# Kernel optimization log

Hardware: AMD Instinct MI355X
Metric: run time of the kernel (lower is better)

The kernel has to match this reference:

```python
import jax, jax.numpy as jnp
import numpy as np

N_NODES = 100000
N_EDGES = 600000
HIDDEN = 128
ALPHA = 0.1
K_HOPS = 10


def setup_inputs() -> dict:
    key = jax.random.key(0)
    k1, k2, k3, k4 = jax.random.split(key, 4)
    x = jax.random.normal(k1, (N_NODES, HIDDEN), dtype=jnp.float32)
    edge_index = jax.random.randint(k2, (2, N_EDGES), 0, N_NODES, dtype=jnp.int64)
    W = jax.random.normal(k3, (HIDDEN, HIDDEN), dtype=jnp.float32) * (1.0 / np.sqrt(HIDDEN))
    b = jax.random.normal(k4, (HIDDEN,), dtype=jnp.float32) * 0.01
    return {"x": x, "edge_index": edge_index, "W": W, "b": b}


def reference(x, edge_index, W, b):
    N = x.shape[0]
    # Linear projection (PyTorch convention: y = x W^T + b)
    h = x @ W.T + b

    # gcn_norm with added self-loops (PyG APPNPConv default)
    loop = jnp.arange(N, dtype=edge_index.dtype)
    src = jnp.concatenate([edge_index[0], loop])  # [E+N]
    dst = jnp.concatenate([edge_index[1], loop])
    ones = jnp.ones(src.shape[0], dtype=h.dtype)
    deg = jax.ops.segment_sum(ones, dst, num_segments=N)  # in-degree incl. self-loop
    dinv = jnp.where(deg > 0, jax.lax.rsqrt(deg), 0.0)
    norm = dinv[src] * dinv[dst]  # [E+N]

    # APPNP propagation: h <- (1-alpha) * A_hat h + alpha * h0
    h0 = h
    for _ in range(K_HOPS):
        msg = norm[:, None] * h[src]  # gather + scale
        agg = jax.ops.segment_sum(msg, dst, num_segments=N)  # scatter-add
        h = (1.0 - ALPHA) * agg + ALPHA * h0
    return h
```

## Files before the change

kernel.cpp:

```cpp
#include <hip/hip_runtime.h>

#define N_NODES_C 100000
#define N_EDGES_C 600000
#define HIDDEN_C 128
#define K_HOPS_C 10
#define SCAN_B 98

typedef short short8 __attribute__((ext_vector_type(8)));
typedef float f32x16 __attribute__((ext_vector_type(16)));

__device__ __forceinline__ unsigned short f2bf(float f) {
    unsigned u = __float_as_uint(f);
    return (unsigned short)((u + 0x7FFFu + ((u >> 16) & 1u)) >> 16);
}
__device__ __forceinline__ float bf_lo(unsigned p) { return __uint_as_float(p << 16); }
__device__ __forceinline__ float bf_hi(unsigned p) { return __uint_as_float(p & 0xFFFF0000u); }

__global__ void k_deg(const int* __restrict__ dst, int* __restrict__ deg, int E) {
    int e = blockIdx.x * blockDim.x + threadIdx.x;
    if (e < E) atomicAdd(&deg[dst[e]], 1);
}

__global__ __launch_bounds__(1024) void k_scan_a(const int* __restrict__ deg,
                                                 int* __restrict__ offs,
                                                 int* __restrict__ blksum,
                                                 float* __restrict__ dinv,
                                                 int* __restrict__ deghist, int N) {
    __shared__ int wtot[16];
    __shared__ int lhist[64];
    int tid = threadIdx.x;
    int i = blockIdx.x * 1024 + tid;
    int lane = tid & 63;
    int wid = tid >> 6;
    if (tid < 64) lhist[tid] = 0;
    __syncthreads();
    int v = (i < N) ? deg[i] : 0;
    if (i < N) {
        dinv[i] = rsqrtf((float)(v + 1));
        atomicAdd(&lhist[v < 63 ? v : 63], 1);
    }
    int incl = v;
#pragma unroll
    for (int d = 1; d < 64; d <<= 1) {
        int t = __shfl_up(incl, (unsigned)d, 64);
        if (lane >= d) incl += t;
    }
    if (lane == 63) wtot[wid] = incl;
    __syncthreads();
    int woff = 0, btot = 0;
#pragma unroll
    for (int w = 0; w < 16; ++w) {
        int t = wtot[w];
        if (w < wid) woff += t;
        btot += t;
    }
    if (i < N) offs[i] = woff + incl - v;
    if (tid == 0) blksum[blockIdx.x] = btot;
    if (tid < 64 && lhist[tid] != 0) atomicAdd(&deghist[tid], lhist[tid]);
}

__global__ __launch_bounds__(128) void k_scan_b(const int* __restrict__ blksum,
                                                int* __restrict__ blkoff,
                                                int* __restrict__ offs,
                                                const int* __restrict__ deghist,
                                                int* __restrict__ bucketcur,
                                                int NB, int N) {
    __shared__ int wt[2];
    int t = threadIdx.x;
    int lane = t & 63;
    int w = t >> 6;
    int v = (t < NB) ? blksum[t] : 0;
    int incl = v;
#pragma unroll
    for (int d = 1; d < 64; d <<= 1) {
        int s = __shfl_up(incl, (unsigned)d, 64);
        if (lane >= d) incl += s;
    }
    if (lane == 63) wt[w] = incl;
    __syncthreads();
    int excl = incl - v + (w == 1 ? wt[0] : 0);
    if (t < NB) blkoff[t] = excl;
    if (t == 127) offs[N] = wt[0] + wt[1];
    if (w == 0) {
        int hv = deghist[lane];
        int hincl = hv;
#pragma unroll
        for (int d = 1; d < 64; d <<= 1) {
            int s = __shfl_up(hincl, (unsigned)d, 64);
            if (lane >= d) hincl += s;
        }
        bucketcur[lane] = hincl - hv;
    }
}

__global__ __launch_bounds__(1024) void k_scan_c(int* __restrict__ offs,
                                                 int* __restrict__ cursor,
                                                 const int* __restrict__ blkoff,
                                                 const int* __restrict__ deg,
                                                 int* __restrict__ bucketcur,
                                                 int* __restrict__ perm,
                                                 uint2* __restrict__ begend, int N) {
    __shared__ int lcnt[64];
    __shared__ int lbase[64];
    int tid = threadIdx.x;
    int i = blockIdx.x * 1024 + tid;
    if (tid < 64) lcnt[tid] = 0;
    __syncthreads();
    int v = 0, d = 0, b = 0, lpos = 0;
    if (i < N) {
        v = offs[i] + blkoff[blockIdx.x];
        offs[i] = v;
        cursor[i] = v;
        d = deg[i];
        b = d < 63 ? d : 63;
        lpos = atomicAdd(&lcnt[b], 1);
    }
    __syncthreads();
    if (tid < 64) lbase[tid] = (lcnt[tid] != 0) ? atomicAdd(&bucketcur[tid], lcnt[tid]) : 0;
    __syncthreads();
    if (i < N) {
        int pos = lbase[b] + lpos;
        perm[pos] = i;
        begend[pos] = make_uint2((unsigned)v, (unsigned)(v + d));
    }
}

__global__ void k_fill(const int* __restrict__ src, const int* __restrict__ dst,
                       const float* __restrict__ dinv, int* __restrict__ cursor,
                       uint2* __restrict__ csr, int E) {
    int e = blockIdx.x * blockDim.x + threadIdx.x;
    if (e < E) {
        int s = src[e], d = dst[e];
        int pos = atomicAdd(&cursor[d], 1);
        uint2 v;
        v.x = (unsigned)s;
        v.y = __float_as_uint(dinv[s] * dinv[d]);
        csr[pos] = v;
    }
}

__global__ __launch_bounds__(256) void k_gemm(const float* __restrict__ x,
                                              const float* __restrict__ W,
                                              const float* __restrict__ b,
                                              unsigned short* __restrict__ hb, int N) {
    __shared__ unsigned short Wb[HIDDEN_C * HIDDEN_C];
    int tid = threadIdx.x;
#pragma unroll
    for (int i = 0; i < 8; ++i) {
        int c = tid + 256 * i;
        int m = c >> 4;
        int g = c & 15;
        const float4* wsrc = (const float4*)W + m * 32 + g * 2;
        float4 wa = wsrc[0];
        float4 wb = wsrc[1];
        unsigned short t8[8];
        t8[0] = f2bf(wa.x); t8[1] = f2bf(wa.y); t8[2] = f2bf(wa.z); t8[3] = f2bf(wa.w);
        t8[4] = f2bf(wb.x); t8[5] = f2bf(wb.y); t8[6] = f2bf(wb.z); t8[7] = f2bf(wb.w);
        int gs = g ^ (m & 15);
        *(uint4*)&Wb[m * 128 + gs * 8] = *(const uint4*)t8;
    }
    __syncthreads();

    int lane = tid & 63;
    int wv = tid >> 6;
    int row0 = blockIdx.x * 128 + wv * 32;
    int m = lane & 31;
    int half = lane >> 5;

    int row = row0 + m;
    if (row >= N) row = N - 1;
    const float4* xrow = (const float4*)(x + (size_t)row * 128);

    f32x16 acc[4];
#pragma unroll
    for (int t = 0; t < 4; ++t)
#pragma unroll
        for (int r = 0; r < 16; ++r) acc[t][r] = 0.f;

    for (int s = 0; s < 8; ++s) {
        int kb = s * 16 + half * 8;
        float4 x0 = xrow[kb >> 2];
        float4 x1 = xrow[(kb >> 2) + 1];
        union { unsigned short u[8]; short8 v; } af;
        af.u[0] = f2bf(x0.x); af.u[1] = f2bf(x0.y); af.u[2] = f2bf(x0.z); af.u[3] = f2bf(x0.w);
        af.u[4] = f2bf(x1.x); af.u[5] = f2bf(x1.y); af.u[6] = f2bf(x1.z); af.u[7] = f2bf(x1.w);
        int g = kb >> 3;
#pragma unroll
        for (int t = 0; t < 4; ++t) {
            int r = t * 32 + m;
            short8 bfrag = *(const short8*)&Wb[r * 128 + ((g ^ (r & 15)) << 3)];
            acc[t] = __builtin_amdgcn_mfma_f32_32x32x16_bf16(af.v, bfrag, acc[t], 0, 0, 0);
        }
    }

    float bias[4];
#pragma unroll
    for (int t = 0; t < 4; ++t) bias[t] = b[t * 32 + m];
#pragma unroll
    for (int t = 0; t < 4; ++t) {
#pragma unroll
        for (int r = 0; r < 16; ++r) {
            int rrow = (r & 3) + 8 * (r >> 2) + 4 * half;
            int node = row0 + rrow;
            if (node < N) {
                float v = acc[t][r] + bias[t];
                hb[(size_t)node * 128 + t * 32 + m] = f2bf(v);
            }
        }
    }
}

__global__ __launch_bounds__(256) void k_prop(const uint4* __restrict__ hin4,
                                              const uint4* __restrict__ h04,
                                              uint4* __restrict__ hout_b,
                                              float* __restrict__ hout_f,
                                              const int* __restrict__ perm,
                                              const uint2* __restrict__ begend,
                                              const uint2* __restrict__ csr,
                                              const float* __restrict__ dinv,
                                              int N, int final_hop) {
    int tid = threadIdx.x;
    int lane = tid & 63;
    int wid = tid >> 6;
    int q = lane >> 4;
    int f = lane & 15;

    int slot = (blockIdx.x * 4 + wid) * 4 + q;
    bool valid = slot < N;

    int node = 0, beg = 0, end = 0;
    if (valid) {
        node = perm[slot];
        uint2 be = begend[slot];
        beg = (int)be.x;
        end = (int)be.y;
    }

    uint4 hq = make_uint4(0u, 0u, 0u, 0u);
    uint4 ps = make_uint4(0u, 0u, 0u, 0u);
    float ws = 0.f;
    if (valid) {
        hq = h04[(size_t)node * 16 + f];
        ps = hin4[(size_t)node * 16 + f];
        float dv = dinv[node];
        ws = dv * dv;
    }

    float acc[8];
#pragma unroll
    for (int i = 0; i < 8; ++i) acc[i] = 0.f;

    int j = beg;
#pragma unroll 2
    for (; j + 2 <= end; j += 2) {
        uint2 e0 = csr[j];
        uint2 e1 = csr[j + 1];
        uint4 p0 = hin4[(size_t)e0.x * 16 + f];
        uint4 p1 = hin4[(size_t)e1.x * 16 + f];
        float w0 = __uint_as_float(e0.y);
        float w1 = __uint_as_float(e1.y);
        acc[0] += w0 * bf_lo(p0.x); acc[1] += w0 * bf_hi(p0.x);
        acc[2] += w0 * bf_lo(p0.y); acc[3] += w0 * bf_hi(p0.y);
        acc[4] += w0 * bf_lo(p0.z); acc[5] += w0 * bf_hi(p0.z);
        acc[6] += w0 * bf_lo(p0.w); acc[7] += w0 * bf_hi(p0.w);
        acc[0] += w1 * bf_lo(p1.x); acc[1] += w1 * bf_hi(p1.x);
        acc[2] += w1 * bf_lo(p1.y); acc[3] += w1 * bf_hi(p1.y);
        acc[4] += w1 * bf_lo(p1.z); acc[5] += w1 * bf_hi(p1.z);
        acc[6] += w1 * bf_lo(p1.w); acc[7] += w1 * bf_hi(p1.w);
    }
    if (j < end) {
        uint2 e = csr[j];
        uint4 p = hin4[(size_t)e.x * 16 + f];
        float w = __uint_as_float(e.y);
        acc[0] += w * bf_lo(p.x); acc[1] += w * bf_hi(p.x);
        acc[2] += w * bf_lo(p.y); acc[3] += w * bf_hi(p.y);
        acc[4] += w * bf_lo(p.z); acc[5] += w * bf_hi(p.z);
        acc[6] += w * bf_lo(p.w); acc[7] += w * bf_hi(p.w);
    }

    acc[0] += ws * bf_lo(ps.x); acc[1] += ws * bf_hi(ps.x);
    acc[2] += ws * bf_lo(ps.y); acc[3] += ws * bf_hi(ps.y);
    acc[4] += ws * bf_lo(ps.z); acc[5] += ws * bf_hi(ps.z);
    acc[6] += ws * bf_lo(ps.w); acc[7] += ws * bf_hi(ps.w);

    if (valid) {
        float o[8];
        o[0] = 0.9f * acc[0] + 0.1f * bf_lo(hq.x);
        o[1] = 0.9f * acc[1] + 0.1f * bf_hi(hq.x);
        o[2] = 0.9f * acc[2] + 0.1f * bf_lo(hq.y);
        o[3] = 0.9f * acc[3] + 0.1f * bf_hi(hq.y);
        o[4] = 0.9f * acc[4] + 0.1f * bf_lo(hq.z);
        o[5] = 0.9f * acc[5] + 0.1f * bf_hi(hq.z);
        o[6] = 0.9f * acc[6] + 0.1f * bf_lo(hq.w);
        o[7] = 0.9f * acc[7] + 0.1f * bf_hi(hq.w);
        if (final_hop) {
            float4* dst0 = (float4*)(hout_f + (size_t)node * 128 + f * 8);
            float4 v0; v0.x = o[0]; v0.y = o[1]; v0.z = o[2]; v0.w = o[3];
            float4 v1; v1.x = o[4]; v1.y = o[5]; v1.z = o[6]; v1.w = o[7];
            dst0[0] = v0;
            dst0[1] = v1;
        } else {
            uint4 p;
            p.x = (unsigned)f2bf(o[0]) | ((unsigned)f2bf(o[1]) << 16);
            p.y = (unsigned)f2bf(o[2]) | ((unsigned)f2bf(o[3]) << 16);
            p.z = (unsigned)f2bf(o[4]) | ((unsigned)f2bf(o[5]) << 16);
            p.w = (unsigned)f2bf(o[6]) | ((unsigned)f2bf(o[7]) << 16);
            hout_b[(size_t)node * 16 + f] = p;
        }
    }
}

extern "C" void kernel_launch(void* const* d_in, const int* in_sizes, int n_in,
                              void* d_out, int out_size, void* d_ws, size_t ws_size,
                              hipStream_t stream) {
    const float* x = (const float*)d_in[0];
    const int* edge = (const int*)d_in[1];
    const float* W = (const float*)d_in[2];
    const float* b = (const float*)d_in[3];
    float* out = (float*)d_out;

    const int N = N_NODES_C;
    const int E = N_EDGES_C;
    const int* src = edge;
    const int* dst = edge + E;

    char* ws = (char*)d_ws;
    size_t off = 0;
    auto carve = [&](size_t bytes) -> void* {
        void* p = ws + off;
        off = (off + bytes + 511) & ~(size_t)511;
        return p;
    };
    unsigned short* h0b = (unsigned short*)carve((size_t)N * HIDDEN_C * 2);
    unsigned short* bA  = (unsigned short*)carve((size_t)N * HIDDEN_C * 2);
    unsigned short* bB  = (unsigned short*)carve((size_t)N * HIDDEN_C * 2);
    int*   deg     = (int*)  carve(((size_t)N + 64) * sizeof(int));
    int*   deghist = deg + N;
    float* dinv    = (float*)carve((size_t)N * sizeof(float));
    int*   offs    = (int*)  carve((size_t)(N + 1) * sizeof(int));
    int*   cursor  = (int*)  carve((size_t)N * sizeof(int));
    uint2* csr     = (uint2*)carve((size_t)E * sizeof(uint2));
    int*   blksum  = (int*)  carve((size_t)SCAN_B * sizeof(int));
    int*   blkoff  = (int*)  carve((size_t)SCAN_B * sizeof(int));
    int*   bucketcur = (int*)carve(64 * sizeof(int));
    int*   perm    = (int*)  carve((size_t)N * sizeof(int));
    uint2* begend  = (uint2*)carve((size_t)N * sizeof(uint2));
    (void)ws_size;

    hipMemsetAsync(deg, 0, ((size_t)N + 64) * sizeof(int), stream);

    int eb = (E + 255) / 256;
    k_deg<<<eb, 256, 0, stream>>>(dst, deg, E);
    k_scan_a<<<SCAN_B, 1024, 0, stream>>>(deg, offs, blksum, dinv, deghist, N);
    k_scan_b<<<1, 128, 0, stream>>>(blksum, blkoff, offs, deghist, bucketcur, SCAN_B, N);
    k_scan_c<<<SCAN_B, 1024, 0, stream>>>(offs, cursor, blkoff, deg, bucketcur, perm, begend, N);
    k_fill<<<eb, 256, 0, stream>>>(src, dst, dinv, cursor, csr, E);

    k_gemm<<<(N + 127) / 128, 256, 0, stream>>>(x, W, b, h0b, N);

    const uint4* hin = (const uint4*)h0b;
    for (int k = 0; k < K_HOPS_C; ++k) {
        int fin = (k == K_HOPS_C - 1);
        uint4* houtb = ((k & 1) == 0) ? (uint4*)bA : (uint4*)bB;
        k_prop<<<(N + 15) / 16, 256, 0, stream>>>(hin, (const uint4*)h0b,
                                                  fin ? nullptr : houtb,
                                                  fin ? out : nullptr,
                                                  perm, begend, csr, dinv, N, fin);
        hin = houtb;
    }
}
```

Baseline: 524.8 us.

## Record per-edge rank during degree count, pack node metadata, unroll gather by four

The degree-count kernel now keeps the atomic return value as each edge's rank within its destination. The CSR fill then computes positions as offs[dst]+rank, so the second round of atomics and the cursor array are no longer needed. The perm, begend and dinv reads in the propagation kernel are merged into one uint4 metadata load per node that carries the self-loop weight precomputed. The edge-gather loop now handles four edges per iteration with clamped indices and zero weights instead of a tail loop. This adds more loads in flight and a little wasted work on short rows, and it stores a 2-byte rank per edge.

Result: faster. 499.0 us, median of 2 (-4.9%).

```diff
diff --git a/kernel.cpp b/kernel.cpp
--- a/kernel.cpp
+++ b/kernel.cpp
@@ -16,9 +16,13 @@
 __device__ __forceinline__ float bf_lo(unsigned p) { return __uint_as_float(p << 16); }
 __device__ __forceinline__ float bf_hi(unsigned p) { return __uint_as_float(p & 0xFFFF0000u); }
 
-__global__ void k_deg(const int* __restrict__ dst, int* __restrict__ deg, int E) {
+__global__ void k_deg(const int* __restrict__ dst, int* __restrict__ deg,
+                      unsigned short* __restrict__ rank, int E) {
     int e = blockIdx.x * blockDim.x + threadIdx.x;
-    if (e < E) atomicAdd(&deg[dst[e]], 1);
+    if (e < E) {
+        int r = atomicAdd(&deg[dst[e]], 1);
+        rank[e] = (unsigned short)r;
+    }
 }
 
 __global__ __launch_bounds__(1024) void k_scan_a(const int* __restrict__ deg,
@@ -94,12 +98,11 @@
 }
 
 __global__ __launch_bounds__(1024) void k_scan_c(int* __restrict__ offs,
-                                                 int* __restrict__ cursor,
                                                  const int* __restrict__ blkoff,
                                                  const int* __restrict__ deg,
+                                                 const float* __restrict__ dinv,
                                                  int* __restrict__ bucketcur,
-                                                 int* __restrict__ perm,
-                                                 uint2* __restrict__ begend, int N) {
+                                                 uint4* __restrict__ meta, int N) {
     __shared__ int lcnt[64];
     __shared__ int lbase[64];
     int tid = threadIdx.x;
@@ -110,7 +113,6 @@
     if (i < N) {
         v = offs[i] + blkoff[blockIdx.x];
         offs[i] = v;
-        cursor[i] = v;
         d = deg[i];
         b = d < 63 ? d : 63;
         lpos = atomicAdd(&lcnt[b], 1);
@@ -120,18 +122,20 @@
     __syncthreads();
     if (i < N) {
         int pos = lbase[b] + lpos;
-        perm[pos] = i;
-        begend[pos] = make_uint2((unsigned)v, (unsigned)(v + d));
+        float dv = dinv[i];
+        meta[pos] = make_uint4((unsigned)v, (unsigned)(v + d), (unsigned)i,
+                               __float_as_uint(dv * dv));
     }
 }
 
 __global__ void k_fill(const int* __restrict__ src, const int* __restrict__ dst,
-                       const float* __restrict__ dinv, int* __restrict__ cursor,
+                       const unsigned short* __restrict__ rank,
+                       const float* __restrict__ dinv, const int* __restrict__ offs,
                        uint2* __restrict__ csr, int E) {
     int e = blockIdx.x * blockDim.x + threadIdx.x;
     if (e < E) {
         int s = src[e], d = dst[e];
-        int pos = atomicAdd(&cursor[d], 1);
+        int pos = offs[d] + (int)rank[e];
         uint2 v;
         v.x = (unsigned)s;
         v.y = __float_as_uint(dinv[s] * dinv[d]);
@@ -214,10 +218,8 @@
                                               const uint4* __restrict__ h04,
                                               uint4* __restrict__ hout_b,
                                               float* __restrict__ hout_f,
-                                              const int* __restrict__ perm,
-                                              const uint2* __restrict__ begend,
+                                              const uint4* __restrict__ meta,
                                               const uint2* __restrict__ csr,
-                                              const float* __restrict__ dinv,
                                               int N, int final_hop) {
     int tid = threadIdx.x;
     int lane = tid & 63;
@@ -229,36 +231,43 @@
     bool valid = slot < N;
 
     int node = 0, beg = 0, end = 0;
+    float ws = 0.f;
     if (valid) {
-        node = perm[slot];
-        uint2 be = begend[slot];
-        beg = (int)be.x;
-        end = (int)be.y;
+        uint4 m = meta[slot];
+        beg = (int)m.x;
+        end = (int)m.y;
+        node = (int)m.z;
+        ws = __uint_as_float(m.w);
     }
 
     uint4 hq = make_uint4(0u, 0u, 0u, 0u);
     uint4 ps = make_uint4(0u, 0u, 0u, 0u);
-    float ws = 0.f;
     if (valid) {
         hq = h04[(size_t)node * 16 + f];
         ps = hin4[(size_t)node * 16 + f];
-        float dv = dinv[node];
-        ws = dv * dv;
     }
 
     float acc[8];
 #pragma unroll
     for (int i = 0; i < 8; ++i) acc[i] = 0.f;
 
-    int j = beg;
 #pragma unroll 2
-    for (; j + 2 <= end; j += 2) {
+    for (int j = beg; j < end; j += 4) {
+        int j1 = (j + 1 < end) ? j + 1 : j;
+        int j2 = (j + 2 < end) ? j + 2 : j;
+        int j3 = (j + 3 < end) ? j + 3 : j;
         uint2 e0 = csr[j];
-        uint2 e1 = csr[j + 1];
+        uint2 e1 = csr[j1];
+        uint2 e2 = csr[j2];
+        uint2 e3 = csr[j3];
         uint4 p0 = hin4[(size_t)e0.x * 16 + f];
         uint4 p1 = hin4[(size_t)e1.x * 16 + f];
+        uint4 p2 = hin4[(size_t)e2.x * 16 + f];
+        uint4 p3 = hin4[(size_t)e3.x * 16 + f];
         float w0 = __uint_as_float(e0.y);
-        float w1 = __uint_as_float(e1.y);
+        float w1 = (j + 1 < end) ? __uint_as_float(e1.y) : 0.f;
+        float w2 = (j + 2 < end) ? __uint_as_float(e2.y) : 0.f;
+        float w3 = (j + 3 < end) ? __uint_as_float(e3.y) : 0.f;
         acc[0] += w0 * bf_lo(p0.x); acc[1] += w0 * bf_hi(p0.x);
         acc[2] += w0 * bf_lo(p0.y); acc[3] += w0 * bf_hi(p0.y);
         acc[4] += w0 * bf_lo(p0.z); acc[5] += w0 * bf_hi(p0.z);
@@ -267,15 +276,14 @@
         acc[2] += w1 * bf_lo(p1.y); acc[3] += w1 * bf_hi(p1.y);
         acc[4] += w1 * bf_lo(p1.z); acc[5] += w1 * bf_hi(p1.z);
         acc[6] += w1 * bf_lo(p1.w); acc[7] += w1 * bf_hi(p1.w);
-    }
-    if (j < end) {
-        uint2 e = csr[j];
-        uint4 p = hin4[(size_t)e.x * 16 + f];
-        float w = __uint_as_float(e.y);
-        acc[0] += w * bf_lo(p.x); acc[1] += w * bf_hi(p.x);
-        acc[2] += w * bf_lo(p.y); acc[3] += w * bf_hi(p.y);
-        acc[4] += w * bf_lo(p.z); acc[5] += w * bf_hi(p.z);
-        acc[6] += w * bf_lo(p.w); acc[7] += w * bf_hi(p.w);
+        acc[0] += w2 * bf_lo(p2.x); acc[1] += w2 * bf_hi(p2.x);
+        acc[2] += w2 * bf_lo(p2.y); acc[3] += w2 * bf_hi(p2.y);
+        acc[4] += w2 * bf_lo(p2.z); acc[5] += w2 * bf_hi(p2.z);
+        acc[6] += w2 * bf_lo(p2.w); acc[7] += w2 * bf_hi(p2.w);
+        acc[0] += w3 * bf_lo(p3.x); acc[1] += w3 * bf_hi(p3.x);
+        acc[2] += w3 * bf_lo(p3.y); acc[3] += w3 * bf_hi(p3.y);
+        acc[4] += w3 * bf_lo(p3.z); acc[5] += w3 * bf_hi(p3.z);
+        acc[6] += w3 * bf_lo(p3.w); acc[7] += w3 * bf_hi(p3.w);
     }
 
     acc[0] += ws * bf_lo(ps.x); acc[1] += ws * bf_hi(ps.x);
@@ -338,23 +346,22 @@
     int*   deghist = deg + N;
     float* dinv    = (float*)carve((size_t)N * sizeof(float));
     int*   offs    = (int*)  carve((size_t)(N + 1) * sizeof(int));
-    int*   cursor  = (int*)  carve((size_t)N * sizeof(int));
+    unsigned short* rank = (unsigned short*)carve((size_t)E * sizeof(unsigned short));
     uint2* csr     = (uint2*)carve((size_t)E * sizeof(uint2));
     int*   blksum  = (int*)  carve((size_t)SCAN_B * sizeof(int));
     int*   blkoff  = (int*)  carve((size_t)SCAN_B * sizeof(int));
     int*   bucketcur = (int*)carve(64 * sizeof(int));
-    int*   perm    = (int*)  carve((size_t)N * sizeof(int));
-    uint2* begend  = (uint2*)carve((size_t)N * sizeof(uint2));
+    uint4* meta    = (uint4*)carve((size_t)N * sizeof(uint4));
     (void)ws_size;
 
     hipMemsetAsync(deg, 0, ((size_t)N + 64) * sizeof(int), stream);
 
     int eb = (E + 255) / 256;
-    k_deg<<<eb, 256, 0, stream>>>(dst, deg, E);
+    k_deg<<<eb, 256, 0, stream>>>(dst, deg, rank, E);
     k_scan_a<<<SCAN_B, 1024, 0, stream>>>(deg, offs, blksum, dinv, deghist, N);
     k_scan_b<<<1, 128, 0, stream>>>(blksum, blkoff, offs, deghist, bucketcur, SCAN_B, N);
-    k_scan_c<<<SCAN_B, 1024, 0, stream>>>(offs, cursor, blkoff, deg, bucketcur, perm, begend, N);
-    k_fill<<<eb, 256, 0, stream>>>(src, dst, dinv, cursor, csr, E);
+    k_scan_c<<<SCAN_B, 1024, 0, stream>>>(offs, blkoff, deg, dinv, bucketcur, meta, N);
+    k_fill<<<eb, 256, 0, stream>>>(src, dst, rank, dinv, offs, csr, E);
 
     k_gemm<<<(N + 127) / 128, 256, 0, stream>>>(x, W, b, h0b, N);
 
@@ -365,7 +372,7 @@
         k_prop<<<(N + 15) / 16, 256, 0, stream>>>(hin, (const uint4*)h0b,
                                                   fin ? nullptr : houtb,
                                                   fin ? out : nullptr,
-                                                  perm, begend, csr, dinv, N, fin);
+                                                  meta, csr, N, fin);
         hin = houtb;
     }
 }
```
